# Kernel tuning notes

Measured on AMD Instinct MI355X. Metric: run time of the kernel, lower is better.

## Reference

```python
import jax, jax.numpy as jnp
import numpy as np
from jax import lax

# Module constraint: hidden_dim == state_dim == expand_dim (see broadcasting in original).
H = 128  # hidden_dim
N = 128  # state_dim
E = 128  # expand_dim = hidden_dim * expand_factor (expand_factor=1)
B, L = 4, 1024


def setup_inputs() -> dict:
    key = jax.random.key(0)
    ks = jax.random.split(key, 11)
    s = lambda fan: 1.0 / np.sqrt(fan)
    return {
        "u": jax.random.normal(ks[0], (B, L, H), jnp.float32),
        "W_in": jax.random.normal(ks[1], (H, 2 * E), jnp.float32) * s(H),
        "b_in": jax.random.normal(ks[2], (2 * E,), jnp.float32) * 0.01,
        "conv_w": jax.random.normal(ks[3], (E, 1, 3), jnp.float32) * s(3),
        "conv_b": jax.random.normal(ks[4], (E,), jnp.float32) * 0.01,
        "W_x": jax.random.normal(ks[5], (E, N + N + H), jnp.float32) * s(E),
        "b_x": jax.random.normal(ks[6], (N + N + H,), jnp.float32) * 0.01,
        "A_log": jax.random.normal(ks[7], (N,), jnp.float32),
        "D": jnp.ones((H,), jnp.float32),
        "W_out": jax.random.normal(ks[8], (E, H), jnp.float32) * s(E),
        "b_out": jax.random.normal(ks[9], (H,), jnp.float32) * 0.01,
    }


def reference(u, W_in, b_in, conv_w, conv_b, W_x, b_x, A_log, D, W_out, b_out):
    b, l, _ = u.shape
    xz = u @ W_in + b_in                       # [B,L,2E]
    x, z = jnp.split(xz, 2, axis=-1)           # [B,L,E] each
    # depthwise conv1d, kernel 3, padding 1 (groups == channels)
    xc = lax.conv_general_dilated(
        x.transpose(0, 2, 1), conv_w, window_strides=(1,), padding=[(1, 1)],
        feature_group_count=E, dimension_numbers=("NCH", "OIH", "NCH"))
    x = jax.nn.silu(xc.transpose(0, 2, 1) + conv_b)  # [B,L,E]
    ssm = x @ W_x + b_x                        # [B,L,2N+H]
    delta = jax.nn.softplus(ssm[..., :N])      # [B,L,N]
    Bm = ssm[..., N:2 * N]                     # [B,L,N]
    C = ssm[..., 2 * N:]                       # [B,L,H]
    A = -jnp.exp(A_log)                        # [N]

    def step(h, inp):
        d_t, B_t, C_t, x_t, u_t = inp          # [B,N],[B,N],[B,H],[B,E],[B,H]
        # A_discrete[b,t,i,j] = exp(delta[b,t,i] * A[j])  (outer broadcast, as in source)
        A_disc = jnp.exp(d_t[:, :, None] * A[None, None, :])       # [B,N,N]
        h = A_disc * h + (d_t * B_t)[:, :, None] * x_t[:, None, :]  # [B,N,E]
        y = (h * C_t[:, None, :]).sum(axis=1) + D * u_t             # [B,H]
        return h, y

    h0 = jnp.zeros((b, N, H), u.dtype)
    inputs = (delta.transpose(1, 0, 2), Bm.transpose(1, 0, 2),
              C.transpose(1, 0, 2), x.transpose(1, 0, 2), u.transpose(1, 0, 2))
    _, ys = lax.scan(step, h0, inputs)         # ys: [L,B,H]
    y = ys.transpose(1, 0, 2) * jax.nn.silu(z)  # [B,L,H] (E==H)
    return y @ W_out + b_out                   # dropout in eval mode: identity
```

## Files before the change

### kernel.cpp

```cpp
#include <hip/hip_runtime.h>
#include <hip/hip_bf16.h>

using bf16 = __hip_bfloat16;
typedef __attribute__((ext_vector_type(8))) short short8;
typedef __attribute__((ext_vector_type(4))) float f32x4;

#define BVAL 4
#define LVAL 1024
#define LOG2E 1.44269504f

#define TSEG 64
#define SSEG 16
#define JW 8
#define CH 16
#define PTS3 76

#define OFF_U      0
#define OFF_WIN    524288
#define OFF_BIN    557056
#define OFF_CONVW  557312
#define OFF_CONVB  557696
#define OFF_WX     557824
#define OFF_BX     606976
#define OFF_ALOG   607360
#define OFF_D      607488
#define OFF_WOUT   607616
#define OFF_BOUT   624000
#define CVT_TOTAL  624128

__device__ __forceinline__ int dtype_flag(const void* D) {
    return ((*(const unsigned int*)D) & 0xFFFFu) != 0u ? 1 : 0;
}
__device__ __forceinline__ float ldin(const void* p, int i, int f) {
    return f ? __bfloat162float(((const bf16*)p)[i]) : ((const float*)p)[i];
}

__global__ void kcvt(const void* __restrict__ u, const void* __restrict__ W_in,
                     const void* __restrict__ b_in, const void* __restrict__ conv_w,
                     const void* __restrict__ conv_b, const void* __restrict__ W_x,
                     const void* __restrict__ b_x, const void* __restrict__ A_log,
                     const void* __restrict__ D, const void* __restrict__ W_out,
                     const void* __restrict__ b_out, float* __restrict__ dst) {
    int idx = blockIdx.x * 256 + threadIdx.x;
    if (idx >= CVT_TOTAL) return;
    int f = dtype_flag(D);
    const void* p; int loc;
    if      (idx < OFF_WIN)   { p = u;      loc = idx; }
    else if (idx < OFF_BIN)   { p = W_in;   loc = idx - OFF_WIN; }
    else if (idx < OFF_CONVW) { p = b_in;   loc = idx - OFF_BIN; }
    else if (idx < OFF_CONVB) { p = conv_w; loc = idx - OFF_CONVW; }
    else if (idx < OFF_WX)    { p = conv_b; loc = idx - OFF_CONVB; }
    else if (idx < OFF_BX)    { p = W_x;    loc = idx - OFF_WX; }
    else if (idx < OFF_ALOG)  { p = b_x;    loc = idx - OFF_BX; }
    else if (idx < OFF_D)     { p = A_log;  loc = idx - OFF_ALOG; }
    else if (idx < OFF_WOUT)  { p = D;      loc = idx - OFF_D; }
    else if (idx < OFF_BOUT)  { p = W_out;  loc = idx - OFF_WOUT; }
    else                      { p = b_out;  loc = idx - OFF_BOUT; }
    dst[idx] = f ? __bfloat162float(((const bf16*)p)[loc]) : ((const float*)p)[loc];
}

#define CVT2_U   524288
#define CVT2_WI  (CVT2_U + 32768)
#define CVT2_WX  (CVT2_WI + 49152)
#define CVT2_TOT (CVT2_WX + 16384)
__global__ void kcvt2(const void* __restrict__ u, const void* __restrict__ W_in,
                      const void* __restrict__ W_x, const void* __restrict__ W_out,
                      const void* __restrict__ D,
                      bf16* __restrict__ ubf, bf16* __restrict__ wtin,
                      bf16* __restrict__ wtx, bf16* __restrict__ wtout) {
    int idx = blockIdx.x * 256 + threadIdx.x;
    if (idx >= CVT2_TOT) return;
    int f = dtype_flag(D);
    if (idx < CVT2_U) {
        ubf[idx] = __float2bfloat16(ldin(u, idx, f));
    } else if (idx < CVT2_WI) {
        int rel = idx - CVT2_U; int n = rel >> 7, k = rel & 127;
        wtin[rel] = __float2bfloat16(ldin(W_in, k * 256 + n, f));
    } else if (idx < CVT2_WX) {
        int rel = idx - CVT2_WI; int n = rel >> 7, k = rel & 127;
        wtx[rel] = __float2bfloat16(ldin(W_x, k * 384 + n, f));
    } else {
        int rel = idx - CVT2_WX; int n = rel >> 7, k = rel & 127;
        wtout[rel] = __float2bfloat16(ldin(W_out, k * 128 + n, f));
    }
}

__global__ void k1_mfma(const bf16* __restrict__ ubf, const bf16* __restrict__ wtin,
                        const float* __restrict__ cvt,
                        float* __restrict__ x_pre, float* __restrict__ zs) {
    int blk = blockIdx.x, mb = blk >> 3, cb = blk & 7;
    int tid = threadIdx.x, w = tid >> 6, lane = tid & 63;
    int quad = lane >> 4, sub = lane & 15;
    int m0 = mb * 64 + w * 16, c = cb * 16;
    f32x4 accX = {0.f, 0.f, 0.f, 0.f}, accZ = {0.f, 0.f, 0.f, 0.f};
    #pragma unroll
    for (int ks = 0; ks < 4; ++ks) {
        int k0 = ks * 32 + quad * 8;
        short8 a  = *(const short8*)(ubf + (size_t)(m0 + sub) * 128 + k0);
        short8 bX = *(const short8*)(wtin + (size_t)(c + sub) * 128 + k0);
        short8 bZ = *(const short8*)(wtin + (size_t)(128 + c + sub) * 128 + k0);
        accX = __builtin_amdgcn_mfma_f32_16x16x32_bf16(a, bX, accX, 0, 0, 0);
        accZ = __builtin_amdgcn_mfma_f32_16x16x32_bf16(a, bZ, accZ, 0, 0, 0);
    }
    int o = c + sub;
    float bx_ = cvt[OFF_BIN + o], bz_ = cvt[OFF_BIN + 128 + o];
    #pragma unroll
    for (int r = 0; r < 4; ++r) {
        int m = m0 + quad * 4 + r;
        float x = accX[r] + bx_;
        float z = accZ[r] + bz_;
        x_pre[(size_t)m * 128 + o] = x;
        zs[(size_t)m * 128 + o] = z / (1.0f + __expf(-z));
    }
}

__global__ void k2_conv(const float* __restrict__ cvt, const float* __restrict__ x_pre,
                        float* __restrict__ xs, bf16* __restrict__ xsbf) {
    const float* conv_w = cvt + OFF_CONVW;
    const float* conv_b = cvt + OFF_CONVB;
    int q = blockIdx.x * 256 + threadIdx.x;
    int basee = q * 4;
    int row = basee >> 7;
    int l = row & (LVAL - 1);
    int e = basee & 127;
    float4 xc = *(const float4*)(x_pre + basee);
    float4 xm = make_float4(0.f, 0.f, 0.f, 0.f);
    float4 xp = make_float4(0.f, 0.f, 0.f, 0.f);
    if (l > 0)        xm = *(const float4*)(x_pre + basee - 128);
    if (l < LVAL - 1) xp = *(const float4*)(x_pre + basee + 128);
    float mm[4] = {xm.x, xm.y, xm.z, xm.w};
    float cc[4] = {xc.x, xc.y, xc.z, xc.w};
    float pp[4] = {xp.x, xp.y, xp.z, xp.w};
    float out[4];
    #pragma unroll
    for (int i = 0; i < 4; ++i) {
        float w0 = conv_w[(e + i) * 3 + 0];
        float w1 = conv_w[(e + i) * 3 + 1];
        float w2 = conv_w[(e + i) * 3 + 2];
        float v = fmaf(w0, mm[i], fmaf(w1, cc[i], fmaf(w2, pp[i], conv_b[e + i])));
        out[i] = v / (1.0f + __expf(-v));
    }
    *(float4*)(xs + basee) = make_float4(out[0], out[1], out[2], out[3]);
    #pragma unroll
    for (int i = 0; i < 4; ++i) xsbf[basee + i] = __float2bfloat16(out[i]);
}

__global__ void k3_mfma(const bf16* __restrict__ xsbf, const bf16* __restrict__ wtx,
                        const float* __restrict__ cvt,
                        float* __restrict__ delta, float* __restrict__ dB,
                        float* __restrict__ Cc) {
    int blk = blockIdx.x, mb = blk >> 3, cb = blk & 7;
    int tid = threadIdx.x, w = tid >> 6, lane = tid & 63;
    int quad = lane >> 4, sub = lane & 15;
    int m0 = mb * 64 + w * 16, c = cb * 16;
    f32x4 accA = {0.f,0.f,0.f,0.f}, accB = {0.f,0.f,0.f,0.f}, accC = {0.f,0.f,0.f,0.f};
    #pragma unroll
    for (int ks = 0; ks < 4; ++ks) {
        int k0 = ks * 32 + quad * 8;
        short8 a  = *(const short8*)(xsbf + (size_t)(m0 + sub) * 128 + k0);
        short8 bA = *(const short8*)(wtx + (size_t)(c + sub) * 128 + k0);
        short8 bB = *(const short8*)(wtx + (size_t)(128 + c + sub) * 128 + k0);
        short8 bC = *(const short8*)(wtx + (size_t)(256 + c + sub) * 128 + k0);
        accA = __builtin_amdgcn_mfma_f32_16x16x32_bf16(a, bA, accA, 0, 0, 0);
        accB = __builtin_amdgcn_mfma_f32_16x16x32_bf16(a, bB, accB, 0, 0, 0);
        accC = __builtin_amdgcn_mfma_f32_16x16x32_bf16(a, bC, accC, 0, 0, 0);
    }
    int o = c + sub;
    float ba = cvt[OFF_BX + o], bb = cvt[OFF_BX + 128 + o], bc = cvt[OFF_BX + 256 + o];
    #pragma unroll
    for (int r = 0; r < 4; ++r) {
        int m = m0 + quad * 4 + r;
        size_t idx = (size_t)m * 128 + o;
        float d = accA[r] + ba;
        float sp = (d > 20.0f) ? d : log1pf(__expf(d));
        delta[idx] = sp;
        dB[idx] = sp * (accB[r] + bb);
        Cc[idx] = accC[r] + bc;
    }
}

__global__ __launch_bounds__(512, 8)
void k5a(const float* __restrict__ cvt, const float* __restrict__ delta,
         const float* __restrict__ dB, const float* __restrict__ xs,
         float* __restrict__ hout, float* __restrict__ Pout) {
    __shared__ float sdl[CH * 128], swl[CH * 128];
    __shared__ float sx[TSEG][JW];
    int blk = blockIdx.x;
    int b = blk >> 8, s = (blk >> 4) & 15, jg = blk & 15;
    int tid = threadIdx.x, w = tid >> 6, lane = tid & 63;
    int j = jg * JW + w;
    int t0 = s * TSEG;
    size_t base = (size_t)b * LVAL * 128;
    {
        int tt = tid >> 3, jj = tid & 7;
        sx[tt][jj] = xs[base + (size_t)(t0 + tt) * 128 + jg * JW + jj];
    }
    float a2 = -__expf(cvt[OFF_ALOG + j]) * LOG2E;
    float h0 = 0.f, h1 = 0.f, p0 = 1.f, p1 = 1.f;
    const float4* gd4 = (const float4*)(delta + base);
    const float4* gw4 = (const float4*)(dB + base);
    for (int c4 = 0; c4 < TSEG / CH; ++c4) {
        __syncthreads();
        int fb = (t0 + c4 * CH) * 32;
        ((float4*)sdl)[tid] = gd4[fb + tid];
        ((float4*)swl)[tid] = gw4[fb + tid];
        __syncthreads();
        #pragma unroll 8
        for (int k = 0; k < CH; ++k) {
            float2 dd = *(const float2*)&sdl[k * 128 + 2 * lane];
            float2 ww = *(const float2*)&swl[k * 128 + 2 * lane];
            float e0 = exp2f(dd.x * a2), e1 = exp2f(dd.y * a2);
            float xv = sx[c4 * CH + k][w];
            h0 = fmaf(e0, h0, ww.x * xv);
            h1 = fmaf(e1, h1, ww.y * xv);
            p0 *= e0; p1 *= e1;
        }
    }
    size_t cidx = (((size_t)(b * SSEG + s) * 128 + j) * 128) + 2 * lane;
    *(float2*)(hout + cidx) = make_float2(h0, h1);
    *(float2*)(Pout + cidx) = make_float2(p0, p1);
}

__global__ void k5b(const float* __restrict__ hout, const float* __restrict__ Pout,
                    float* __restrict__ hin) {
    int c = blockIdx.x * 2 + (threadIdx.x >> 6);
    int lane = threadIdx.x & 63;
    int b = c >> 7, j = c & 127;
    float h0 = 0.f, h1 = 0.f;
    #pragma unroll
    for (int s = 0; s < SSEG; ++s) {
        size_t idx = (((size_t)(b * SSEG + s) * 128 + j) * 128) + 2 * lane;
        *(float2*)(hin + idx) = make_float2(h0, h1);
        float2 ho = *(const float2*)(hout + idx);
        float2 pp = *(const float2*)(Pout + idx);
        h0 = fmaf(pp.x, h0, ho.x);
        h1 = fmaf(pp.y, h1, ho.y);
    }
}

__global__ __launch_bounds__(512, 8)
void k5c(const float* __restrict__ cvt, const float* __restrict__ delta,
         const float* __restrict__ dB, const float* __restrict__ Cc,
         const float* __restrict__ xs, const float* __restrict__ zs,
         const float* __restrict__ hin, bf16* __restrict__ y2bf) {
    __shared__ float sdl[CH * 128], swl[CH * 128];
    __shared__ float sx[TSEG][JW], sc[TSEG][JW], su[TSEG][JW], sz[TSEG][JW];
    __shared__ float pt[JW][8 * PTS3];
    int blk = blockIdx.x;
    int b = blk >> 8, s = (blk >> 4) & 15, jg = blk & 15;
    int tid = threadIdx.x, w = tid >> 6, lane = tid & 63;
    int j = jg * JW + w;
    int t0 = s * TSEG;
    size_t base = (size_t)b * LVAL * 128;
    {
        int tt = tid >> 3, jj = tid & 7;
        size_t g = base + (size_t)(t0 + tt) * 128 + jg * JW + jj;
        sx[tt][jj] = xs[g];
        sc[tt][jj] = Cc[g];
        su[tt][jj] = cvt[OFF_U + g];
        sz[tt][jj] = zs[g];
    }
    float a2 = -__expf(cvt[OFF_ALOG + j]) * LOG2E;
    float Dj = cvt[OFF_D + j];
    size_t cidx = (((size_t)(b * SSEG + s) * 128 + j) * 128) + 2 * lane;
    float2 hh = *(const float2*)(hin + cidx);
    float h0 = hh.x, h1 = hh.y;
    const float4* gd4 = (const float4*)(delta + base);
    const float4* gw4 = (const float4*)(dB + base);
    float* ptw = pt[w];
    int t_r = lane >> 3, g8 = lane & 7;
    for (int c4 = 0; c4 < TSEG / CH; ++c4) {
        __syncthreads();
        int fb = (t0 + c4 * CH) * 32;
        ((float4*)sdl)[tid] = gd4[fb + tid];
        ((float4*)swl)[tid] = gw4[fb + tid];
        __syncthreads();
        for (int cb = 0; cb < CH / 8; ++cb) {
            #pragma unroll
            for (int k = 0; k < 8; ++k) {
                int kk = cb * 8 + k;
                float2 dd = *(const float2*)&sdl[kk * 128 + 2 * lane];
                float2 ww = *(const float2*)&swl[kk * 128 + 2 * lane];
                float xv = sx[c4 * CH + kk][w];
                h0 = fmaf(exp2f(dd.x * a2), h0, ww.x * xv);
                h1 = fmaf(exp2f(dd.y * a2), h1, ww.y * xv);
                ptw[k * PTS3 + lane] = h0 + h1;
            }
            const float4* pr = (const float4*)&ptw[t_r * PTS3 + g8 * 8];
            float4 v0 = pr[0], v1 = pr[1];
            float sum = ((v0.x + v0.y) + (v0.z + v0.w)) + ((v1.x + v1.y) + (v1.z + v1.w));
            sum += __shfl_xor(sum, 1, 64);
            sum += __shfl_xor(sum, 2, 64);
            sum += __shfl_xor(sum, 4, 64);
            if (g8 == 0) {
                int tt = c4 * CH + cb * 8 + t_r;
                float y = fmaf(sc[tt][w], sum, Dj * su[tt][w]);
                y2bf[base + (size_t)(t0 + tt) * 128 + j] =
                    __float2bfloat16(y * sz[tt][w]);
            }
        }
    }
}

__global__ void k6_mfma(const bf16* __restrict__ y2bf, const bf16* __restrict__ wtout,
                        const float* __restrict__ cvt, const void* __restrict__ Din,
                        void* __restrict__ out) {
    int blk = blockIdx.x, mb = blk >> 2, nb = blk & 3;
    int tid = threadIdx.x, w = tid >> 6, lane = tid & 63;
    int quad = lane >> 4, sub = lane & 15;
    int m0 = mb * 64 + w * 16, n0 = nb * 32;
    f32x4 acc0 = {0.f,0.f,0.f,0.f}, acc1 = {0.f,0.f,0.f,0.f};
    #pragma unroll
    for (int ks = 0; ks < 4; ++ks) {
        int k0 = ks * 32 + quad * 8;
        short8 a  = *(const short8*)(y2bf + (size_t)(m0 + sub) * 128 + k0);
        short8 b0 = *(const short8*)(wtout + (size_t)(n0 + sub) * 128 + k0);
        short8 b1 = *(const short8*)(wtout + (size_t)(n0 + 16 + sub) * 128 + k0);
        acc0 = __builtin_amdgcn_mfma_f32_16x16x32_bf16(a, b0, acc0, 0, 0, 0);
        acc1 = __builtin_amdgcn_mfma_f32_16x16x32_bf16(a, b1, acc1, 0, 0, 0);
    }
    int f = dtype_flag(Din);
    float bo0 = cvt[OFF_BOUT + n0 + sub], bo1 = cvt[OFF_BOUT + n0 + 16 + sub];
    #pragma unroll
    for (int r = 0; r < 4; ++r) {
        int m = m0 + quad * 4 + r;
        float v0 = acc0[r] + bo0, v1 = acc1[r] + bo1;
        if (f) {
            ((bf16*)out)[(size_t)m * 128 + n0 + sub] = __float2bfloat16(v0);
            ((bf16*)out)[(size_t)m * 128 + n0 + 16 + sub] = __float2bfloat16(v1);
        } else {
            ((float*)out)[(size_t)m * 128 + n0 + sub] = v0;
            ((float*)out)[(size_t)m * 128 + n0 + 16 + sub] = v1;
        }
    }
}

extern "C" void kernel_launch(void* const* d_in, const int* in_sizes, int n_in,
                              void* d_out, int out_size, void* d_ws, size_t ws_size,
                              hipStream_t stream) {
    const size_t NE = (size_t)BVAL * LVAL * 128;
    const size_t NC = (size_t)BVAL * SSEG * 128 * 128;

    float* cvt   = (float*)d_ws;
    float* bufs  = cvt + CVT_TOTAL;
    float* x_pre = bufs + 0 * NE;
    float* zs    = bufs + 1 * NE;
    float* xs    = bufs + 2 * NE;
    float* delta = bufs + 3 * NE;
    float* dB    = bufs + 4 * NE;
    float* Cc    = bufs + 5 * NE;
    float* hout  = bufs + 6 * NE;
    float* Pou   = hout + NC;
    float* hin   = Pou + NC;
    float* bfarea = hin + NC;
    bf16* ubf   = (bf16*)bfarea;
    bf16* xsbf  = ubf + NE;
    bf16* y2bf  = xsbf + NE;
    bf16* wtin  = y2bf + NE;
    bf16* wtx   = wtin + 32768;
    bf16* wtout = wtx + 49152;

    const int ROWS = BVAL * LVAL;

    kcvt<<<(CVT_TOTAL + 255) / 256, 256, 0, stream>>>(
        d_in[0], d_in[1], d_in[2], d_in[3], d_in[4], d_in[5],
        d_in[6], d_in[7], d_in[8], d_in[9], d_in[10], cvt);
    kcvt2<<<(CVT2_TOT + 255) / 256, 256, 0, stream>>>(
        d_in[0], d_in[1], d_in[5], d_in[9], d_in[8], ubf, wtin, wtx, wtout);
    k1_mfma<<<512, 256, 0, stream>>>(ubf, wtin, cvt, x_pre, zs);
    k2_conv<<<(ROWS * 128) / (256 * 4), 256, 0, stream>>>(cvt, x_pre, xs, xsbf);
    k3_mfma<<<512, 256, 0, stream>>>(xsbf, wtx, cvt, delta, dB, Cc);
    k5a<<<BVAL * SSEG * (128 / JW), 512, 0, stream>>>(cvt, delta, dB, xs, hout, Pou);
    k5b<<<256, 128, 0, stream>>>(hout, Pou, hin);
    k5c<<<BVAL * SSEG * (128 / JW), 512, 0, stream>>>(cvt, delta, dB, Cc, xs, zs, hin, y2bf);
    k6_mfma<<<256, 256, 0, stream>>>(y2bf, wtout, cvt, d_in[8], d_out);
}
```

Before: 153.5 us.

## Fuse conversions and conv into GEMMs, replace segment decay products with delta sums

The two conversion kernels are merged into one that no longer writes a full fp32 copy of u and the large weights. Only the small vectors are kept in fp32. The depthwise conv plus SiLU is folded into the x-projection MFMA kernel, which removes a launch and the xsbf round trip, though each column block now recomputes the conv. The scan's per-segment decay product buffer (B×S×N×N) is replaced by per-segment delta sums (B×S×N), and k5b recomputes the decay with exp2, cutting a large write and read. k5c reads C, z and u per row from global memory instead of staging them in LDS.

```diff
diff --git a/kernel.cpp b/kernel.cpp
--- a/kernel.cpp
+++ b/kernel.cpp
@@ -15,73 +15,64 @@
 #define CH 16
 #define PTS3 76
 
-#define OFF_U      0
-#define OFF_WIN    524288
-#define OFF_BIN    557056
-#define OFF_CONVW  557312
-#define OFF_CONVB  557696
-#define OFF_WX     557824
-#define OFF_BX     606976
-#define OFF_ALOG   607360
-#define OFF_D      607488
-#define OFF_WOUT   607616
-#define OFF_BOUT   624000
-#define CVT_TOTAL  624128
+#define OFF_BIN    0
+#define OFF_CONVW  256
+#define OFF_CONVB  640
+#define OFF_BX     768
+#define OFF_ALOG   1152
+#define OFF_D      1280
+#define OFF_BOUT   1408
+#define CVT_SMALL  1536
+
+#define R_UBF   524288
+#define R_WTIN  (R_UBF + 32768)
+#define R_WTX   (R_WTIN + 49152)
+#define R_WTOUT (R_WTX + 16384)
+#define R_TOT   (R_WTOUT + CVT_SMALL)
 
 __device__ __forceinline__ int dtype_flag(const void* D) {
     return ((*(const unsigned int*)D) & 0xFFFFu) != 0u ? 1 : 0;
 }
-__device__ __forceinline__ float ldin(const void* p, int i, int f) {
+__device__ __forceinline__ float ldin(const void* p, size_t i, int f) {
     return f ? __bfloat162float(((const bf16*)p)[i]) : ((const float*)p)[i];
 }
-
-__global__ void kcvt(const void* __restrict__ u, const void* __restrict__ W_in,
-                     const void* __restrict__ b_in, const void* __restrict__ conv_w,
-                     const void* __restrict__ conv_b, const void* __restrict__ W_x,
-                     const void* __restrict__ b_x, const void* __restrict__ A_log,
-                     const void* __restrict__ D, const void* __restrict__ W_out,
-                     const void* __restrict__ b_out, float* __restrict__ dst) {
+__device__ __forceinline__ short f2bf(float x) {
+    union { bf16 h; short s; } u; u.h = __float2bfloat16(x); return u.s;
+}
+
+__global__ void k0_cvt(const void* __restrict__ u, const void* __restrict__ W_in,
+                       const void* __restrict__ b_in, const void* __restrict__ conv_w,
+                       const void* __restrict__ conv_b, const void* __restrict__ W_x,
+                       const void* __restrict__ b_x, const void* __restrict__ A_log,
+                       const void* __restrict__ D, const void* __restrict__ W_out,
+                       const void* __restrict__ b_out,
+                       float* __restrict__ cvt, bf16* __restrict__ ubf,
+                       bf16* __restrict__ wtin, bf16* __restrict__ wtx,
+                       bf16* __restrict__ wtout) {
     int idx = blockIdx.x * 256 + threadIdx.x;
-    if (idx >= CVT_TOTAL) return;
+    if (idx >= R_TOT) return;
     int f = dtype_flag(D);
-    const void* p; int loc;
-    if      (idx < OFF_WIN)   { p = u;      loc = idx; }
-    else if (idx < OFF_BIN)   { p = W_in;   loc = idx - OFF_WIN; }
-    else if (idx < OFF_CONVW) { p = b_in;   loc = idx - OFF_BIN; }
-    else if (idx < OFF_CONVB) { p = conv_w; loc = idx - OFF_CONVW; }
-    else if (idx < OFF_WX)    { p = conv_b; loc = idx - OFF_CONVB; }
-    else if (idx < OFF_BX)    { p = W_x;    loc = idx - OFF_WX; }
-    else if (idx < OFF_ALOG)  { p = b_x;    loc = idx - OFF_BX; }
-    else if (idx < OFF_D)     { p = A_log;  loc = idx - OFF_ALOG; }
-    else if (idx < OFF_WOUT)  { p = D;      loc = idx - OFF_D; }
-    else if (idx < OFF_BOUT)  { p = W_out;  loc = idx - OFF_WOUT; }
-    else                      { p = b_out;  loc = idx - OFF_BOUT; }
-    dst[idx] = f ? __bfloat162float(((const bf16*)p)[loc]) : ((const float*)p)[loc];
-}
-
-#define CVT2_U   524288
-#define CVT2_WI  (CVT2_U + 32768)
-#define CVT2_WX  (CVT2_WI + 49152)
-#define CVT2_TOT (CVT2_WX + 16384)
-__global__ void kcvt2(const void* __restrict__ u, const void* __restrict__ W_in,
-                      const void* __restrict__ W_x, const void* __restrict__ W_out,
-                      const void* __restrict__ D,
-                      bf16* __restrict__ ubf, bf16* __restrict__ wtin,
-                      bf16* __restrict__ wtx, bf16* __restrict__ wtout) {
-    int idx = blockIdx.x * 256 + threadIdx.x;
-    if (idx >= CVT2_TOT) return;
-    int f = dtype_flag(D);
-    if (idx < CVT2_U) {
+    if (idx < R_UBF) {
         ubf[idx] = __float2bfloat16(ldin(u, idx, f));
-    } else if (idx < CVT2_WI) {
-        int rel = idx - CVT2_U; int n = rel >> 7, k = rel & 127;
-        wtin[rel] = __float2bfloat16(ldin(W_in, k * 256 + n, f));
-    } else if (idx < CVT2_WX) {
-        int rel = idx - CVT2_WI; int n = rel >> 7, k = rel & 127;
-        wtx[rel] = __float2bfloat16(ldin(W_x, k * 384 + n, f));
+    } else if (idx < R_WTIN) {
+        int rel = idx - R_UBF; int n = rel >> 7, k = rel & 127;
+        wtin[rel] = __float2bfloat16(ldin(W_in, (size_t)k * 256 + n, f));
+    } else if (idx < R_WTX) {
+        int rel = idx - R_WTIN; int n = rel >> 7, k = rel & 127;
+        wtx[rel] = __float2bfloat16(ldin(W_x, (size_t)k * 384 + n, f));
+    } else if (idx < R_WTOUT) {
+        int rel = idx - R_WTX; int n = rel >> 7, k = rel & 127;
+        wtout[rel] = __float2bfloat16(ldin(W_out, (size_t)k * 128 + n, f));
     } else {
-        int rel = idx - CVT2_WX; int n = rel >> 7, k = rel & 127;
-        wtout[rel] = __float2bfloat16(ldin(W_out, k * 128 + n, f));
+        int rel = idx - R_WTOUT; const void* p; int loc;
+        if      (rel < 256)  { p = b_in;   loc = rel; }
+        else if (rel < 640)  { p = conv_w; loc = rel - 256; }
+        else if (rel < 768)  { p = conv_b; loc = rel - 640; }
+        else if (rel < 1152) { p = b_x;    loc = rel - 768; }
+        else if (rel < 1280) { p = A_log;  loc = rel - 1152; }
+        else if (rel < 1408) { p = D;      loc = rel - 1280; }
+        else                 { p = b_out;  loc = rel - 1408; }
+        cvt[rel] = ldin(p, loc, f);
     }
 }
 
@@ -114,50 +105,59 @@
     }
 }
 
-__global__ void k2_conv(const float* __restrict__ cvt, const float* __restrict__ x_pre,
-                        float* __restrict__ xs, bf16* __restrict__ xsbf) {
-    const float* conv_w = cvt + OFF_CONVW;
-    const float* conv_b = cvt + OFF_CONVB;
-    int q = blockIdx.x * 256 + threadIdx.x;
-    int basee = q * 4;
-    int row = basee >> 7;
-    int l = row & (LVAL - 1);
-    int e = basee & 127;
-    float4 xc = *(const float4*)(x_pre + basee);
-    float4 xm = make_float4(0.f, 0.f, 0.f, 0.f);
-    float4 xp = make_float4(0.f, 0.f, 0.f, 0.f);
-    if (l > 0)        xm = *(const float4*)(x_pre + basee - 128);
-    if (l < LVAL - 1) xp = *(const float4*)(x_pre + basee + 128);
-    float mm[4] = {xm.x, xm.y, xm.z, xm.w};
-    float cc[4] = {xc.x, xc.y, xc.z, xc.w};
-    float pp[4] = {xp.x, xp.y, xp.z, xp.w};
-    float out[4];
-    #pragma unroll
-    for (int i = 0; i < 4; ++i) {
-        float w0 = conv_w[(e + i) * 3 + 0];
-        float w1 = conv_w[(e + i) * 3 + 1];
-        float w2 = conv_w[(e + i) * 3 + 2];
-        float v = fmaf(w0, mm[i], fmaf(w1, cc[i], fmaf(w2, pp[i], conv_b[e + i])));
-        out[i] = v / (1.0f + __expf(-v));
-    }
-    *(float4*)(xs + basee) = make_float4(out[0], out[1], out[2], out[3]);
-    #pragma unroll
-    for (int i = 0; i < 4; ++i) xsbf[basee + i] = __float2bfloat16(out[i]);
-}
-
-__global__ void k3_mfma(const bf16* __restrict__ xsbf, const bf16* __restrict__ wtx,
-                        const float* __restrict__ cvt,
+__global__ void k3_mfma(const float* __restrict__ x_pre, const bf16* __restrict__ wtx,
+                        const float* __restrict__ cvt, float* __restrict__ xs,
                         float* __restrict__ delta, float* __restrict__ dB,
                         float* __restrict__ Cc) {
+    __shared__ float swc[128 * 4];
     int blk = blockIdx.x, mb = blk >> 3, cb = blk & 7;
     int tid = threadIdx.x, w = tid >> 6, lane = tid & 63;
     int quad = lane >> 4, sub = lane & 15;
+    if (tid < 128) {
+        swc[tid * 4 + 0] = cvt[OFF_CONVW + tid * 3 + 0];
+        swc[tid * 4 + 1] = cvt[OFF_CONVW + tid * 3 + 1];
+        swc[tid * 4 + 2] = cvt[OFF_CONVW + tid * 3 + 2];
+        swc[tid * 4 + 3] = cvt[OFF_CONVB + tid];
+    }
+    __syncthreads();
     int m0 = mb * 64 + w * 16, c = cb * 16;
+    int row = m0 + sub;
+    int l = row & (LVAL - 1);
+    const float* xr = x_pre + (size_t)row * 128;
     f32x4 accA = {0.f,0.f,0.f,0.f}, accB = {0.f,0.f,0.f,0.f}, accC = {0.f,0.f,0.f,0.f};
     #pragma unroll
     for (int ks = 0; ks < 4; ++ks) {
         int k0 = ks * 32 + quad * 8;
-        short8 a  = *(const short8*)(xsbf + (size_t)(m0 + sub) * 128 + k0);
+        float ccv[8], mmv[8], ppv[8];
+        *(float4*)&ccv[0] = *(const float4*)(xr + k0);
+        *(float4*)&ccv[4] = *(const float4*)(xr + k0 + 4);
+        if (l > 0) {
+            *(float4*)&mmv[0] = *(const float4*)(xr + k0 - 128);
+            *(float4*)&mmv[4] = *(const float4*)(xr + k0 - 124);
+        } else {
+            #pragma unroll
+            for (int i = 0; i < 8; ++i) mmv[i] = 0.f;
+        }
+        if (l < LVAL - 1) {
+            *(float4*)&ppv[0] = *(const float4*)(xr + k0 + 128);
+            *(float4*)&ppv[4] = *(const float4*)(xr + k0 + 132);
+        } else {
+            #pragma unroll
+            for (int i = 0; i < 8; ++i) ppv[i] = 0.f;
+        }
+        float o[8];
+        short8 a;
+        #pragma unroll
+        for (int i = 0; i < 8; ++i) {
+            const float* wc = &swc[(k0 + i) * 4];
+            float v = fmaf(wc[0], mmv[i], fmaf(wc[1], ccv[i], fmaf(wc[2], ppv[i], wc[3])));
+            o[i] = v / (1.0f + __expf(-v));
+            a[i] = f2bf(o[i]);
+        }
+        if (cb == 0) {
+            *(float4*)(xs + (size_t)row * 128 + k0)     = *(float4*)&o[0];
+            *(float4*)(xs + (size_t)row * 128 + k0 + 4) = *(float4*)&o[4];
+        }
         short8 bA = *(const short8*)(wtx + (size_t)(c + sub) * 128 + k0);
         short8 bB = *(const short8*)(wtx + (size_t)(128 + c + sub) * 128 + k0);
         short8 bC = *(const short8*)(wtx + (size_t)(256 + c + sub) * 128 + k0);
@@ -182,7 +182,7 @@
 __global__ __launch_bounds__(512, 8)
 void k5a(const float* __restrict__ cvt, const float* __restrict__ delta,
          const float* __restrict__ dB, const float* __restrict__ xs,
-         float* __restrict__ hout, float* __restrict__ Pout) {
+         float* __restrict__ hout, float* __restrict__ Sd) {
     __shared__ float sdl[CH * 128], swl[CH * 128];
     __shared__ float sx[TSEG][JW];
     int blk = blockIdx.x;
@@ -196,7 +196,7 @@
         sx[tt][jj] = xs[base + (size_t)(t0 + tt) * 128 + jg * JW + jj];
     }
     float a2 = -__expf(cvt[OFF_ALOG + j]) * LOG2E;
-    float h0 = 0.f, h1 = 0.f, p0 = 1.f, p1 = 1.f;
+    float h0 = 0.f, h1 = 0.f, sd0 = 0.f, sd1 = 0.f;
     const float4* gd4 = (const float4*)(delta + base);
     const float4* gw4 = (const float4*)(dB + base);
     for (int c4 = 0; c4 < TSEG / CH; ++c4) {
@@ -213,28 +213,31 @@
             float xv = sx[c4 * CH + k][w];
             h0 = fmaf(e0, h0, ww.x * xv);
             h1 = fmaf(e1, h1, ww.y * xv);
-            p0 *= e0; p1 *= e1;
+            sd0 += dd.x; sd1 += dd.y;
         }
     }
     size_t cidx = (((size_t)(b * SSEG + s) * 128 + j) * 128) + 2 * lane;
     *(float2*)(hout + cidx) = make_float2(h0, h1);
-    *(float2*)(Pout + cidx) = make_float2(p0, p1);
-}
-
-__global__ void k5b(const float* __restrict__ hout, const float* __restrict__ Pout,
-                    float* __restrict__ hin) {
+    if (jg == 0 && w == 0) {
+        *(float2*)(Sd + (size_t)(b * SSEG + s) * 128 + 2 * lane) = make_float2(sd0, sd1);
+    }
+}
+
+__global__ void k5b(const float* __restrict__ cvt, const float* __restrict__ hout,
+                    const float* __restrict__ Sd, float* __restrict__ hin) {
     int c = blockIdx.x * 2 + (threadIdx.x >> 6);
     int lane = threadIdx.x & 63;
     int b = c >> 7, j = c & 127;
+    float a2 = -__expf(cvt[OFF_ALOG + j]) * LOG2E;
     float h0 = 0.f, h1 = 0.f;
     #pragma unroll
     for (int s = 0; s < SSEG; ++s) {
         size_t idx = (((size_t)(b * SSEG + s) * 128 + j) * 128) + 2 * lane;
         *(float2*)(hin + idx) = make_float2(h0, h1);
         float2 ho = *(const float2*)(hout + idx);
-        float2 pp = *(const float2*)(Pout + idx);
-        h0 = fmaf(pp.x, h0, ho.x);
-        h1 = fmaf(pp.y, h1, ho.y);
+        float2 sd = *(const float2*)(Sd + (size_t)(b * SSEG + s) * 128 + 2 * lane);
+        h0 = fmaf(exp2f(a2 * sd.x), h0, ho.x);
+        h1 = fmaf(exp2f(a2 * sd.y), h1, ho.y);
     }
 }
 
@@ -242,9 +245,10 @@
 void k5c(const float* __restrict__ cvt, const float* __restrict__ delta,
          const float* __restrict__ dB, const float* __restrict__ Cc,
          const float* __restrict__ xs, const float* __restrict__ zs,
-         const float* __restrict__ hin, bf16* __restrict__ y2bf) {
+         const float* __restrict__ hin, const void* __restrict__ uin,
+         const void* __restrict__ Din, bf16* __restrict__ y2bf) {
     __shared__ float sdl[CH * 128], swl[CH * 128];
-    __shared__ float sx[TSEG][JW], sc[TSEG][JW], su[TSEG][JW], sz[TSEG][JW];
+    __shared__ float sx[TSEG][JW];
     __shared__ float pt[JW][8 * PTS3];
     int blk = blockIdx.x;
     int b = blk >> 8, s = (blk >> 4) & 15, jg = blk & 15;
@@ -252,13 +256,10 @@
     int j = jg * JW + w;
     int t0 = s * TSEG;
     size_t base = (size_t)b * LVAL * 128;
+    int f = dtype_flag(Din);
     {
         int tt = tid >> 3, jj = tid & 7;
-        size_t g = base + (size_t)(t0 + tt) * 128 + jg * JW + jj;
-        sx[tt][jj] = xs[g];
-        sc[tt][jj] = Cc[g];
-        su[tt][jj] = cvt[OFF_U + g];
-        sz[tt][jj] = zs[g];
+        sx[tt][jj] = xs[base + (size_t)(t0 + tt) * 128 + jg * JW + jj];
     }
     float a2 = -__expf(cvt[OFF_ALOG + j]) * LOG2E;
     float Dj = cvt[OFF_D + j];
@@ -276,6 +277,11 @@
         ((float4*)swl)[tid] = gw4[fb + tid];
         __syncthreads();
         for (int cb = 0; cb < CH / 8; ++cb) {
+            int tte = c4 * CH + cb * 8 + t_r;
+            size_t gi = base + (size_t)(t0 + tte) * 128 + j;
+            float cC = Cc[gi];
+            float cz = zs[gi];
+            float cu = ldin(uin, gi, f);
             #pragma unroll
             for (int k = 0; k < 8; ++k) {
                 int kk = cb * 8 + k;
@@ -293,10 +299,8 @@
             sum += __shfl_xor(sum, 2, 64);
             sum += __shfl_xor(sum, 4, 64);
             if (g8 == 0) {
-                int tt = c4 * CH + cb * 8 + t_r;
-                float y = fmaf(sc[tt][w], sum, Dj * su[tt][w]);
-                y2bf[base + (size_t)(t0 + tt) * 128 + j] =
-                    __float2bfloat16(y * sz[tt][w]);
+                float y = fmaf(cC, sum, Dj * cu);
+                y2bf[gi] = __float2bfloat16(y * cz);
             }
         }
     }
@@ -342,7 +346,7 @@
     const size_t NC = (size_t)BVAL * SSEG * 128 * 128;
 
     float* cvt   = (float*)d_ws;
-    float* bufs  = cvt + CVT_TOTAL;
+    float* bufs  = cvt + 2048;
     float* x_pre = bufs + 0 * NE;
     float* zs    = bufs + 1 * NE;
     float* xs    = bufs + 2 * NE;
@@ -350,28 +354,23 @@
     float* dB    = bufs + 4 * NE;
     float* Cc    = bufs + 5 * NE;
     float* hout  = bufs + 6 * NE;
-    float* Pou   = hout + NC;
-    float* hin   = Pou + NC;
-    float* bfarea = hin + NC;
-    bf16* ubf   = (bf16*)bfarea;
-    bf16* xsbf  = ubf + NE;
-    bf16* y2bf  = xsbf + NE;
-    bf16* wtin  = y2bf + NE;
-    bf16* wtx   = wtin + 32768;
-    bf16* wtout = wtx + 49152;
-
-    const int ROWS = BVAL * LVAL;
-
-    kcvt<<<(CVT_TOTAL + 255) / 256, 256, 0, stream>>>(
+    float* hin   = hout + NC;
+    float* Sd    = hin + NC;
+    bf16* ubf    = (bf16*)(Sd + 8192);
+    bf16* y2bf   = ubf + NE;
+    bf16* wtin   = y2bf + NE;
+    bf16* wtx    = wtin + 32768;
+    bf16* wtout  = wtx + 49152;
+
+    k0_cvt<<<(R_TOT + 255) / 256, 256, 0, stream>>>(
         d_in[0], d_in[1], d_in[2], d_in[3], d_in[4], d_in[5],
-        d_in[6], d_in[7], d_in[8], d_in[9], d_in[10], cvt);
-    kcvt2<<<(CVT2_TOT + 255) / 256, 256, 0, stream>>>(
-        d_in[0], d_in[1], d_in[5], d_in[9], d_in[8], ubf, wtin, wtx, wtout);
+        d_in[6], d_in[7], d_in[8], d_in[9], d_in[10],
+        cvt, ubf, wtin, wtx, wtout);
     k1_mfma<<<512, 256, 0, stream>>>(ubf, wtin, cvt, x_pre, zs);
-    k2_conv<<<(ROWS * 128) / (256 * 4), 256, 0, stream>>>(cvt, x_pre, xs, xsbf);
-    k3_mfma<<<512, 256, 0, stream>>>(xsbf, wtx, cvt, delta, dB, Cc);
-    k5a<<<BVAL * SSEG * (128 / JW), 512, 0, stream>>>(cvt, delta, dB, xs, hout, Pou);
-    k5b<<<256, 128, 0, stream>>>(hout, Pou, hin);
-    k5c<<<BVAL * SSEG * (128 / JW), 512, 0, stream>>>(cvt, delta, dB, Cc, xs, zs, hin, y2bf);
+    k3_mfma<<<512, 256, 0, stream>>>(x_pre, wtx, cvt, xs, delta, dB, Cc);
+    k5a<<<BVAL * SSEG * (128 / JW), 512, 0, stream>>>(cvt, delta, dB, xs, hout, Sd);
+    k5b<<<256, 128, 0, stream>>>(cvt, hout, Sd, hin);
+    k5c<<<BVAL * SSEG * (128 / JW), 512, 0, stream>>>(cvt, delta, dB, Cc, xs, zs, hin,
+        d_in[0], d_in[8], y2bf);
     k6_mfma<<<256, 256, 0, stream>>>(y2bf, wtout, cvt, d_in[8], d_out);
 }
```

After: 153.2 us. Within noise of the previous version (-0.2%).
